# Kernel tuning notes

Measured on AMD Instinct MI355X. Metric: run time of the kernel, lower is better.

Reference implementation:

```python
import jax, jax.numpy as jnp
import numpy as np

VOCAB, D = 14848, 128

def setup_inputs() -> dict:
    key = jax.random.key(0)
    ks = jax.random.split(key, 7)
    x = jax.random.randint(ks[0], (65536, 32), 0, VOCAB, dtype=jnp.int32)
    emb = jax.random.normal(ks[1], (VOCAB, D), dtype=jnp.float32) * 0.05
    w2 = jax.random.normal(ks[2], (32, 128), dtype=jnp.float32) * (1.0 / np.sqrt(128))
    b2 = jax.random.normal(ks[3], (32,), dtype=jnp.float32) * 0.01
    w3 = jax.random.normal(ks[4], (32, 64), dtype=jnp.float32) * (1.0 / np.sqrt(64))
    b3 = jax.random.normal(ks[5], (32,), dtype=jnp.float32) * 0.01
    w4 = jax.random.normal(ks[6], (1, 64), dtype=jnp.float32) * (1.0 / np.sqrt(64))
    return {"x": x, "emb": emb, "w2": w2, "b2": b2, "w3": w3, "b3": b3, "w4": w4}

def reference(x, emb, w2, b2, w3, b3, w4):
    idx = x[..., :29]                      # [B, 29]
    h = emb[idx].sum(axis=-2)              # [B, 128] gather + sum accumulator
    h = jax.nn.relu(h)
    h = h @ w2.T + b2                      # [B, 32]
    h = jax.nn.relu(jnp.concatenate((h, -h), axis=-1))  # [B, 64]
    h = h @ w3.T + b3                      # [B, 32]
    h = jax.nn.relu(jnp.concatenate((h, -h), axis=-1))  # [B, 64]
    return h @ w4.T                        # [B, 1]
```

## Files before the change

kernel.cpp:

```cpp
#include <hip/hip_runtime.h>
#include <hip/hip_fp16.h>


#define STR 65

using h2  = _Float16 __attribute__((ext_vector_type(2)));
using h4  = _Float16 __attribute__((ext_vector_type(4)));
using h8v = _Float16 __attribute__((ext_vector_type(8)));

union H8 { h8v v; h2 h[4]; };

__device__ __forceinline__ float frelu(float v) { return v > 0.f ? v : 0.f; }

__device__ __forceinline__ h2 h2relu(h2 v) {
    h2 r;
    r[0] = v[0] > (_Float16)0 ? v[0] : (_Float16)0;
    r[1] = v[1] > (_Float16)0 ? v[1] : (_Float16)0;
    return r;
}

__global__ __launch_bounds__(256) void cvt_emb(const float* __restrict__ emb,
                                               _Float16* __restrict__ tab) {
    const int i = blockIdx.x * 256 + threadIdx.x;
    const float4 v = ((const float4*)emb)[i];
    h4 o;
    o[0] = (_Float16)v.x; o[1] = (_Float16)v.y;
    o[2] = (_Float16)v.z; o[3] = (_Float16)v.w;
    ((h4*)tab)[i] = o;
}

__global__ __launch_bounds__(256) void prep_w(
    const float* __restrict__ w2, const float* __restrict__ w3,
    const float* __restrict__ w4,
    _Float16* __restrict__ w2p, h2* __restrict__ w3p, h2* __restrict__ w4p) {
    const int i = threadIdx.x;
    for (int e = i; e < 32 * 128; e += 256) w2p[e] = (_Float16)w2[e];
    for (int p = i; p < 32 * 32; p += 256) {
        const int o = p >> 5, j = p & 31;
        h2 c; c[0] = (_Float16)w3[o * 64 + j]; c[1] = (_Float16)w3[o * 64 + 32 + j];
        w3p[p] = c;
    }
    if (i < 32) {
        h2 c; c[0] = (_Float16)w4[i]; c[1] = (_Float16)w4[32 + i];
        w4p[i] = c;
    }
}

__global__ __launch_bounds__(256, 4) void nnue_fwd(
    const int* __restrict__ x, const _Float16* __restrict__ tab,
    const h2* __restrict__ w2p, const float* __restrict__ b2,
    const h2* __restrict__ w3p, const float* __restrict__ b3,
    const h2* __restrict__ w4p, float* __restrict__ out)
{
    __shared__ h2 lds[64 * STR];

    const int t    = threadIdx.x;
    const int lane = t & 63;
    const int g    = lane >> 4;
    const int sub  = lane & 15;
    const int row0 = blockIdx.x * 64;
    const int wave = __builtin_amdgcn_readfirstlane(t >> 6);

    for (int it = 0; it < 4; ++it) {
        const int rb = wave * 16 + it * 4;
        const int xv0 = x[(size_t)(row0 + rb + g) * 32 + sub];
        const int xv1 = x[(size_t)(row0 + rb + g) * 32 + 16 + sub];

        h2 accA[4] = {}, accB[4] = {};
        #pragma unroll
        for (int j = 0; j < 29; ++j) {
            const int src = (lane & 48) | (j & 15);
            const int idx = __shfl((j < 16) ? xv0 : xv1, src, 64);
            H8 u;
            u.v = *(const h8v*)((const char*)tab +
                                (((unsigned)idx) << 8) + (sub << 4));
            if (j & 1) {
                accB[0] += u.h[0]; accB[1] += u.h[1];
                accB[2] += u.h[2]; accB[3] += u.h[3];
            } else {
                accA[0] += u.h[0]; accA[1] += u.h[1];
                accA[2] += u.h[2]; accA[3] += u.h[3];
            }
        }
        #pragma unroll
        for (int k = 0; k < 4; ++k) {
            const h2 s = h2relu(accA[k] + accB[k]);
            lds[(4 * sub + k) * STR + rb + g] = s;
        }
    }
    __syncthreads();

    const int r  = lane;
    const int ob = __builtin_amdgcn_readfirstlane((t >> 6) * 8);

    float a2[8];
    #pragma unroll
    for (int oo = 0; oo < 8; ++oo) a2[oo] = b2[ob + oo];
    #pragma unroll 8
    for (int pd = 0; pd < 64; ++pd) {
        const h2 hp = lds[pd * STR + r];
        #pragma unroll
        for (int oo = 0; oo < 8; ++oo)
            a2[oo] = __builtin_amdgcn_fdot2(hp, w2p[(ob + oo) * 64 + pd],
                                            a2[oo], false);
    }
    __syncthreads();
    #pragma unroll
    for (int oo = 0; oo < 8; ++oo) {
        h2 c; c[0] = (_Float16)frelu(a2[oo]); c[1] = (_Float16)frelu(-a2[oo]);
        lds[(ob + oo) * STR + r] = c;
    }
    __syncthreads();

    float a3[8];
    #pragma unroll
    for (int oo = 0; oo < 8; ++oo) a3[oo] = b3[ob + oo];
    #pragma unroll 8
    for (int j = 0; j < 32; ++j) {
        const h2 cp = lds[j * STR + r];
        #pragma unroll
        for (int oo = 0; oo < 8; ++oo)
            a3[oo] = __builtin_amdgcn_fdot2(cp, w3p[(ob + oo) * 32 + j],
                                            a3[oo], false);
    }
    #pragma unroll
    for (int oo = 0; oo < 8; ++oo) {
        h2 c; c[0] = (_Float16)frelu(a3[oo]); c[1] = (_Float16)frelu(-a3[oo]);
        lds[(32 + ob + oo) * STR + r] = c;
    }
    __syncthreads();

    if (t < 64) {
        float s = 0.f;
        #pragma unroll
        for (int j = 0; j < 32; ++j)
            s = __builtin_amdgcn_fdot2(lds[(32 + j) * STR + t], w4p[j], s, false);
        out[row0 + t] = s;
    }
}

extern "C" void kernel_launch(void* const* d_in, const int* in_sizes, int n_in,
                              void* d_out, int out_size, void* d_ws, size_t ws_size,
                              hipStream_t stream) {
    const int*   x   = (const int*)d_in[0];
    const float* emb = (const float*)d_in[1];
    const float* w2  = (const float*)d_in[2];
    const float* b2  = (const float*)d_in[3];
    const float* w3  = (const float*)d_in[4];
    const float* b3  = (const float*)d_in[5];
    const float* w4  = (const float*)d_in[6];
    float* out = (float*)d_out;

    const int emb_elems = in_sizes[1];
    const int n_rows    = in_sizes[0] / 32;

    char* ws = (char*)d_ws;
    _Float16* tab = (_Float16*)ws;
    _Float16* w2p = (_Float16*)(ws + 3801088);
    h2*       w3p = (h2*)(ws + 3801088 + 8192);
    h2*       w4p = (h2*)(ws + 3801088 + 8192 + 4096);

    hipLaunchKernelGGL(cvt_emb, dim3(emb_elems / 4 / 256), dim3(256), 0, stream,
                       emb, tab);
    hipLaunchKernelGGL(prep_w, dim3(1), dim3(256), 0, stream,
                       w2, w3, w4, w2p, w3p, w4p);
    hipLaunchKernelGGL(nnue_fwd, dim3(n_rows / 64), dim3(256), 0, stream,
                       x, tab, (const h2*)w2p, b2, w3p, b3, w4p, out);
}
```

Before: 106.4 us.

## Merge prep kernels into one launch and halve rows per forward block

Combines the embedding conversion and weight preparation into a single staging kernel, with the last block handling the weights, which removes one kernel launch. The forward kernel now processes 32 rows per block instead of 64, doubling the grid and raising the occupancy hint to 8 blocks per CU. In the MLP stages half of each wave now duplicates work on the same 32 rows and only the lower half writes results, so the dense-layer compute per row effectively doubles in exchange for more parallelism during the gather phase.

```diff
diff --git a/kernel.cpp b/kernel.cpp
--- a/kernel.cpp
+++ b/kernel.cpp
@@ -2,7 +2,7 @@
 #include <hip/hip_fp16.h>
 
 
-#define STR 65
+#define STR2 33
 
 using h2  = _Float16 __attribute__((ext_vector_type(2)));
 using h4  = _Float16 __attribute__((ext_vector_type(4)));
@@ -19,8 +19,27 @@
     return r;
 }
 
-__global__ __launch_bounds__(256) void cvt_emb(const float* __restrict__ emb,
-                                               _Float16* __restrict__ tab) {
+__global__ __launch_bounds__(256) void stage(
+    const float* __restrict__ emb, _Float16* __restrict__ tab,
+    const float* __restrict__ w2, const float* __restrict__ w3,
+    const float* __restrict__ w4,
+    _Float16* __restrict__ w2p, h2* __restrict__ w3p, h2* __restrict__ w4p,
+    int n4) {
+    if ((int)blockIdx.x == (int)gridDim.x - 1) {
+        const int i = threadIdx.x;
+        for (int e = i; e < 32 * 128; e += 256) w2p[e] = (_Float16)w2[e];
+        for (int p = i; p < 32 * 32; p += 256) {
+            const int o = p >> 5, j = p & 31;
+            h2 c; c[0] = (_Float16)w3[o * 64 + j];
+            c[1] = (_Float16)w3[o * 64 + 32 + j];
+            w3p[p] = c;
+        }
+        if (i < 32) {
+            h2 c; c[0] = (_Float16)w4[i]; c[1] = (_Float16)w4[32 + i];
+            w4p[i] = c;
+        }
+        return;
+    }
     const int i = blockIdx.x * 256 + threadIdx.x;
     const float4 v = ((const float4*)emb)[i];
     h4 o;
@@ -29,40 +48,24 @@
     ((h4*)tab)[i] = o;
 }
 
-__global__ __launch_bounds__(256) void prep_w(
-    const float* __restrict__ w2, const float* __restrict__ w3,
-    const float* __restrict__ w4,
-    _Float16* __restrict__ w2p, h2* __restrict__ w3p, h2* __restrict__ w4p) {
-    const int i = threadIdx.x;
-    for (int e = i; e < 32 * 128; e += 256) w2p[e] = (_Float16)w2[e];
-    for (int p = i; p < 32 * 32; p += 256) {
-        const int o = p >> 5, j = p & 31;
-        h2 c; c[0] = (_Float16)w3[o * 64 + j]; c[1] = (_Float16)w3[o * 64 + 32 + j];
-        w3p[p] = c;
-    }
-    if (i < 32) {
-        h2 c; c[0] = (_Float16)w4[i]; c[1] = (_Float16)w4[32 + i];
-        w4p[i] = c;
-    }
-}
-
-__global__ __launch_bounds__(256, 4) void nnue_fwd(
+__global__ __launch_bounds__(256, 8) void nnue_fwd(
     const int* __restrict__ x, const _Float16* __restrict__ tab,
     const h2* __restrict__ w2p, const float* __restrict__ b2,
     const h2* __restrict__ w3p, const float* __restrict__ b3,
     const h2* __restrict__ w4p, float* __restrict__ out)
 {
-    __shared__ h2 lds[64 * STR];
+    __shared__ h2 lds[64 * STR2];
 
     const int t    = threadIdx.x;
     const int lane = t & 63;
     const int g    = lane >> 4;
     const int sub  = lane & 15;
-    const int row0 = blockIdx.x * 64;
+    const int row0 = blockIdx.x * 32;
     const int wave = __builtin_amdgcn_readfirstlane(t >> 6);
 
-    for (int it = 0; it < 4; ++it) {
-        const int rb = wave * 16 + it * 4;
+    #pragma unroll
+    for (int it = 0; it < 2; ++it) {
+        const int rb = wave * 8 + it * 4;
         const int xv0 = x[(size_t)(row0 + rb + g) * 32 + sub];
         const int xv1 = x[(size_t)(row0 + rb + g) * 32 + 16 + sub];
 
@@ -85,12 +88,13 @@
         #pragma unroll
         for (int k = 0; k < 4; ++k) {
             const h2 s = h2relu(accA[k] + accB[k]);
-            lds[(4 * sub + k) * STR + rb + g] = s;
+            lds[(4 * sub + k) * STR2 + rb + g] = s;
         }
     }
     __syncthreads();
 
-    const int r  = lane;
+    const int r  = lane & 31;
+    const int hf = lane >> 5;
     const int ob = __builtin_amdgcn_readfirstlane((t >> 6) * 8);
 
     float a2[8];
@@ -98,17 +102,19 @@
     for (int oo = 0; oo < 8; ++oo) a2[oo] = b2[ob + oo];
     #pragma unroll 8
     for (int pd = 0; pd < 64; ++pd) {
-        const h2 hp = lds[pd * STR + r];
+        const h2 hp = lds[pd * STR2 + r];
         #pragma unroll
         for (int oo = 0; oo < 8; ++oo)
             a2[oo] = __builtin_amdgcn_fdot2(hp, w2p[(ob + oo) * 64 + pd],
                                             a2[oo], false);
     }
     __syncthreads();
-    #pragma unroll
-    for (int oo = 0; oo < 8; ++oo) {
-        h2 c; c[0] = (_Float16)frelu(a2[oo]); c[1] = (_Float16)frelu(-a2[oo]);
-        lds[(ob + oo) * STR + r] = c;
+    if (hf == 0) {
+        #pragma unroll
+        for (int oo = 0; oo < 8; ++oo) {
+            h2 c; c[0] = (_Float16)frelu(a2[oo]); c[1] = (_Float16)frelu(-a2[oo]);
+            lds[(ob + oo) * STR2 + r] = c;
+        }
     }
     __syncthreads();
 
@@ -117,24 +123,26 @@
     for (int oo = 0; oo < 8; ++oo) a3[oo] = b3[ob + oo];
     #pragma unroll 8
     for (int j = 0; j < 32; ++j) {
-        const h2 cp = lds[j * STR + r];
+        const h2 cp = lds[j * STR2 + r];
         #pragma unroll
         for (int oo = 0; oo < 8; ++oo)
             a3[oo] = __builtin_amdgcn_fdot2(cp, w3p[(ob + oo) * 32 + j],
                                             a3[oo], false);
     }
-    #pragma unroll
-    for (int oo = 0; oo < 8; ++oo) {
-        h2 c; c[0] = (_Float16)frelu(a3[oo]); c[1] = (_Float16)frelu(-a3[oo]);
-        lds[(32 + ob + oo) * STR + r] = c;
+    if (hf == 0) {
+        #pragma unroll
+        for (int oo = 0; oo < 8; ++oo) {
+            h2 c; c[0] = (_Float16)frelu(a3[oo]); c[1] = (_Float16)frelu(-a3[oo]);
+            lds[(32 + ob + oo) * STR2 + r] = c;
+        }
     }
     __syncthreads();
 
-    if (t < 64) {
+    if (t < 32) {
         float s = 0.f;
         #pragma unroll
         for (int j = 0; j < 32; ++j)
-            s = __builtin_amdgcn_fdot2(lds[(32 + j) * STR + t], w4p[j], s, false);
+            s = __builtin_amdgcn_fdot2(lds[(32 + j) * STR2 + t], w4p[j], s, false);
         out[row0 + t] = s;
     }
 }
@@ -153,6 +161,7 @@
 
     const int emb_elems = in_sizes[1];
     const int n_rows    = in_sizes[0] / 32;
+    const int n4        = emb_elems / 4;
 
     char* ws = (char*)d_ws;
     _Float16* tab = (_Float16*)ws;
@@ -160,10 +169,8 @@
     h2*       w3p = (h2*)(ws + 3801088 + 8192);
     h2*       w4p = (h2*)(ws + 3801088 + 8192 + 4096);
 
-    hipLaunchKernelGGL(cvt_emb, dim3(emb_elems / 4 / 256), dim3(256), 0, stream,
-                       emb, tab);
-    hipLaunchKernelGGL(prep_w, dim3(1), dim3(256), 0, stream,
-                       w2, w3, w4, w2p, w3p, w4p);
-    hipLaunchKernelGGL(nnue_fwd, dim3(n_rows / 64), dim3(256), 0, stream,
+    hipLaunchKernelGGL(stage, dim3(n4 / 256 + 1), dim3(256), 0, stream,
+                       emb, tab, w2, w3, w4, w2p, w3p, w4p, n4);
+    hipLaunchKernelGGL(nnue_fwd, dim3(n_rows / 32), dim3(256), 0, stream,
                        x, tab, (const h2*)w2p, b2, w3p, b3, w4p, out);
 }
```

New measurement: 105.5 us. Within noise of the previous version (-0.9%).
